# Optimization experiments

Measured on AMD Instinct MI355X. Metric: run time of the kernel, lower is better.

Reference implementation:

```python
import jax, jax.numpy as jnp
import numpy as np

T = 16384       # video length (frames)
C = 7           # out_features = d_model = num surgical phases
F_DIM = 2048    # mstcn_f_dim (spatial feature dim)
LEN_Q = 30      # sliding window length
N_HEADS = 4
D_K = 64        # attn_dim = min(64, mstcn_f_maps=64)
D_FF = 64       # d_ff = mstcn_f_maps


def setup_inputs() -> dict:
    key = jax.random.key(0)
    ks = jax.random.split(key, 10)
    w = lambda i, shape: jax.random.normal(ks[i], shape, jnp.float32) * 0.05
    return {
        "x": jax.random.normal(ks[0], (1, C, T), jnp.float32),
        "long_feature": jax.random.normal(ks[1], (1, T, F_DIM), jnp.float32),
        "W_fc": w(2, (C, F_DIM)),              # nn.Linear(mstcn_f_dim, out_features, bias=False)
        "W_q": w(3, (N_HEADS * D_K, C)),
        "W_k": w(4, (N_HEADS * D_K, C)),
        "W_v": w(5, (N_HEADS * D_K, C)),
        "W_o": w(6, (C, N_HEADS * D_K)),
        "ln1_g": jnp.ones((C,), jnp.float32),
        "ln1_b": jnp.zeros((C,), jnp.float32),
        "W_ff1": w(7, (D_FF, C)),
        "W_ff2": w(8, (C, D_FF)),
        "ln2_g": jnp.ones((C,), jnp.float32),
        "ln2_b": jnp.zeros((C,), jnp.float32),
    }


def layer_norm(x, g, b, eps=1e-5):
    mu = x.mean(-1, keepdims=True)
    var = ((x - mu) ** 2).mean(-1, keepdims=True)
    return (x - mu) * jax.lax.rsqrt(var + eps) * g + b


def reference(x, long_feature, W_fc, W_q, W_k, W_v, W_o, ln1_g, ln1_b, W_ff1, W_ff2, ln2_g, ln2_b):
    # --- vectorized sliding-window (replaces the Python loop of zeros/cat/stack) ---
    feats = x[0].T                                            # (T, C)
    padded = jnp.concatenate([jnp.zeros((LEN_Q - 1, C), feats.dtype), feats], axis=0)
    idx = jnp.arange(T)[:, None] + jnp.arange(LEN_Q)[None, :]  # window ends at frame i
    inputs = padded[idx]                                       # (T, LEN_Q, C)

    # --- spatial embedding: feas = tanh(fc(long_feature)).transpose(0,1) ---
    feas = jnp.tanh(long_feature[0] @ W_fc.T)[:, None, :]      # (T, 1, C)

    # --- decoder layer: cross MHA(query=feas, kv=inputs) + residual + LN ---
    q = (feas @ W_q.T).reshape(T, 1, N_HEADS, D_K).transpose(0, 2, 1, 3)       # (T,H,1,Dk)
    k = (inputs @ W_k.T).reshape(T, LEN_Q, N_HEADS, D_K).transpose(0, 2, 1, 3)  # (T,H,Lq,Dk)
    v = (inputs @ W_v.T).reshape(T, LEN_Q, N_HEADS, D_K).transpose(0, 2, 1, 3)  # (T,H,Lq,Dk)
    scores = jnp.einsum('thqd,thkd->thqk', q, k) / np.float32(np.sqrt(D_K))
    attn = jax.nn.softmax(scores, axis=-1)
    ctx = jnp.einsum('thqk,thkd->thqd', attn, v)
    ctx = ctx.transpose(0, 2, 1, 3).reshape(T, 1, N_HEADS * D_K)
    out = layer_norm(ctx @ W_o.T + feas, ln1_g, ln1_b)         # (T, 1, C)

    # --- position-wise FFN + residual + LN ---
    ff = jax.nn.relu(out @ W_ff1.T) @ W_ff2.T
    out = layer_norm(ff + out, ln2_g, ln2_b)
    return out[:, 0]                                           # (T, C) per-frame logits
```

## Files before the change

### kernel.cpp

```cpp
#include <hip/hip_runtime.h>
#include <math.h>

#define T_FRAMES 16384
#define FDIM 2048
#define LQ 30

__global__ __launch_bounds__(448) void setup_kernel(
    const float* __restrict__ Wq, const float* __restrict__ Wk,
    const float* __restrict__ Wv, const float* __restrict__ Wo,
    float* __restrict__ AM) {
  const int e = threadIdx.x;
  if (e >= 392) return;
  const int which = e / 196;
  const int r = e % 196;
  const int h = r / 49;
  const int rr = r % 49;
  const int c = rr / 7;
  const int c2 = rr % 7;
  float s = 0.0f;
  if (which == 0) {
    for (int d = 0; d < 64; ++d)
      s = fmaf(Wq[(h * 64 + d) * 7 + c], Wk[(h * 64 + d) * 7 + c2], s);
  } else {
    for (int d = 0; d < 64; ++d)
      s = fmaf(Wo[c * 256 + h * 64 + d], Wv[(h * 64 + d) * 7 + c2], s);
  }
  AM[e] = s;
}

#define FPB_A 8

__global__ __launch_bounds__(256) void feas_kernel(
    const float* __restrict__ lf,
    const float* __restrict__ Wfc,
    float* __restrict__ feas) {
  const int tid = threadIdx.x;
  const int lane = tid & 63;
  const int wave = tid >> 6;
  const int t0 = blockIdx.x * FPB_A + wave * 2;
  const float* lfp = lf + (size_t)t0 * FDIM + lane * 4;

  float4 a0[8], a1[8];
#pragma unroll
  for (int ch = 0; ch < 8; ++ch) a0[ch] = *(const float4*)(lfp + ch * 256);
#pragma unroll
  for (int ch = 0; ch < 8; ++ch) a1[ch] = *(const float4*)(lfp + FDIM + ch * 256);

  float acc0[7] = {0, 0, 0, 0, 0, 0, 0};
  float acc1[7] = {0, 0, 0, 0, 0, 0, 0};
#pragma unroll
  for (int ch = 0; ch < 8; ++ch) {
#pragma unroll
    for (int c = 0; c < 7; ++c) {
      const float4 w = *(const float4*)(Wfc + c * FDIM + ch * 256 + lane * 4);
      acc0[c] = fmaf(a0[ch].x, w.x, fmaf(a0[ch].y, w.y,
                fmaf(a0[ch].z, w.z, fmaf(a0[ch].w, w.w, acc0[c]))));
      acc1[c] = fmaf(a1[ch].x, w.x, fmaf(a1[ch].y, w.y,
                fmaf(a1[ch].z, w.z, fmaf(a1[ch].w, w.w, acc1[c]))));
    }
  }

#pragma unroll
  for (int c = 0; c < 7; ++c) {
    float v0 = acc0[c];
    float v1 = acc1[c];
#pragma unroll
    for (int off = 32; off > 0; off >>= 1) {
      v0 += __shfl_down(v0, off, 64);
      v1 += __shfl_down(v1, off, 64);
    }
    if (lane == 0) {
      feas[(size_t)t0 * 7 + c]       = tanhf(v0);
      feas[(size_t)(t0 + 1) * 7 + c] = tanhf(v1);
    }
  }
}

#define BF 64

__global__ __launch_bounds__(256) void attn_kernel(
    const float* __restrict__ x,
    const float* __restrict__ feas_g,
    const float* __restrict__ AM,
    const float* __restrict__ W1,
    const float* __restrict__ W2,
    const float* __restrict__ ln1g, const float* __restrict__ ln1b,
    const float* __restrict__ ln2g, const float* __restrict__ ln2b,
    float* __restrict__ out) {
  __shared__ float AM_s[392];
  __shared__ float ft[(BF + LQ - 1) * 7];
  __shared__ float feas_s[BF][7];
  __shared__ float hpart[BF][4][7];

  const int tid = threadIdx.x;
  const int t0 = blockIdx.x * BF;

  for (int i = tid; i < 392; i += 256) AM_s[i] = AM[i];
  for (int i = tid; i < (BF + LQ - 1) * 7; i += 256) {
    const int row = i / 7, c = i % 7;
    const int s = t0 - (LQ - 1) + row;
    ft[i] = (s >= 0) ? x[c * T_FRAMES + s] : 0.0f;
  }
  for (int i = tid; i < BF * 7; i += 256)
    feas_s[i / 7][i % 7] = feas_g[(size_t)t0 * 7 + i];
  __syncthreads();

  {
    const int f = tid >> 2;
    const int h = tid & 3;
    float fe[7];
#pragma unroll
    for (int c = 0; c < 7; ++c) fe[c] = feas_s[f][c];

    const float* Ah = AM_s + h * 49;
    const float* Mh = AM_s + 196 + h * 49;
    float qk[7];
#pragma unroll
    for (int c2 = 0; c2 < 7; ++c2) {
      float s = 0.0f;
#pragma unroll
      for (int c = 0; c < 7; ++c) s = fmaf(fe[c], Ah[c * 7 + c2], s);
      qk[c2] = s * 0.125f;
    }
    const float* frow = &ft[f * 7];
    float sc[LQ];
    float m = -1e30f;
#pragma unroll
    for (int j = 0; j < LQ; ++j) {
      const float* r = frow + j * 7;
      float s = 0.0f;
#pragma unroll
      for (int c2 = 0; c2 < 7; ++c2) s = fmaf(qk[c2], r[c2], s);
      sc[j] = s;
      m = fmaxf(m, s);
    }
    float sum = 0.0f;
    float wsum[7] = {0, 0, 0, 0, 0, 0, 0};
#pragma unroll
    for (int j = 0; j < LQ; ++j) {
      const float p = __expf(sc[j] - m);
      sum += p;
      const float* r = frow + j * 7;
#pragma unroll
      for (int c2 = 0; c2 < 7; ++c2) wsum[c2] = fmaf(p, r[c2], wsum[c2]);
    }
    const float inv = 1.0f / sum;
#pragma unroll
    for (int c = 0; c < 7; ++c) {
      float s = 0.0f;
#pragma unroll
      for (int c2 = 0; c2 < 7; ++c2) s = fmaf(Mh[c * 7 + c2], wsum[c2], s);
      hpart[f][h][c] = s * inv;
    }
  }
  __syncthreads();

  if (tid < BF) {
    const int f = tid;
    float v[7];
#pragma unroll
    for (int c = 0; c < 7; ++c)
      v[c] = feas_s[f][c] + hpart[f][0][c] + hpart[f][1][c] + hpart[f][2][c] + hpart[f][3][c];

    float mu = 0.0f;
#pragma unroll
    for (int c = 0; c < 7; ++c) mu += v[c];
    mu *= (1.0f / 7.0f);
    float var = 0.0f;
#pragma unroll
    for (int c = 0; c < 7; ++c) { const float d = v[c] - mu; var = fmaf(d, d, var); }
    var *= (1.0f / 7.0f);
    float rs = rsqrtf(var + 1e-5f);
    float o1[7];
#pragma unroll
    for (int c = 0; c < 7; ++c) o1[c] = (v[c] - mu) * rs * ln1g[c] + ln1b[c];

    float ff[7] = {0, 0, 0, 0, 0, 0, 0};
    for (int k = 0; k < 64; ++k) {
      float hk = 0.0f;
#pragma unroll
      for (int c = 0; c < 7; ++c) hk = fmaf(W1[k * 7 + c], o1[c], hk);
      hk = fmaxf(hk, 0.0f);
#pragma unroll
      for (int c = 0; c < 7; ++c) ff[c] = fmaf(W2[c * 64 + k], hk, ff[c]);
    }

#pragma unroll
    for (int c = 0; c < 7; ++c) v[c] = ff[c] + o1[c];
    mu = 0.0f;
#pragma unroll
    for (int c = 0; c < 7; ++c) mu += v[c];
    mu *= (1.0f / 7.0f);
    var = 0.0f;
#pragma unroll
    for (int c = 0; c < 7; ++c) { const float d = v[c] - mu; var = fmaf(d, d, var); }
    var *= (1.0f / 7.0f);
    rs = rsqrtf(var + 1e-5f);
    const int t = t0 + f;
#pragma unroll
    for (int c = 0; c < 7; ++c)
      out[(size_t)t * 7 + c] = (v[c] - mu) * rs * ln2g[c] + ln2b[c];
  }
}

extern "C" void kernel_launch(void* const* d_in, const int* in_sizes, int n_in,
                              void* d_out, int out_size, void* d_ws, size_t ws_size,
                              hipStream_t stream) {
  const float* x    = (const float*)d_in[0];
  const float* lf   = (const float*)d_in[1];
  const float* Wfc  = (const float*)d_in[2];
  const float* Wq   = (const float*)d_in[3];
  const float* Wk   = (const float*)d_in[4];
  const float* Wv   = (const float*)d_in[5];
  const float* Wo   = (const float*)d_in[6];
  const float* ln1g = (const float*)d_in[7];
  const float* ln1b = (const float*)d_in[8];
  const float* W1   = (const float*)d_in[9];
  const float* W2   = (const float*)d_in[10];
  const float* ln2g = (const float*)d_in[11];
  const float* ln2b = (const float*)d_in[12];
  float* out = (float*)d_out;

  float* AM = (float*)d_ws;

  setup_kernel<<<1, 448, 0, stream>>>(Wq, Wk, Wv, Wo, AM);
  feas_kernel<<<T_FRAMES / FPB_A, 256, 0, stream>>>(lf, Wfc, out);
  attn_kernel<<<T_FRAMES / BF, 256, 0, stream>>>(
      x, out, AM, W1, W2, ln1g, ln1b, ln2g, ln2b, out);
}
```

Measured before the change: 277.3 us.

## Fuse feature projection into attention kernel with Wfc staged in LDS

Merges the long-feature projection kernel into the attention/FFN kernel. Each block of 32 frames now computes its own tanh(fc) features into shared memory, which removes the global round-trip of feas and one kernel launch. The 57KB Wfc matrix is copied into LDS per block instead of being read from global/L2 by every wave. The trade-off is that the large LDS allocation limits occupancy, and each of the 512 blocks reloads Wfc, on a kernel that is bound by HBM streaming of long_feature.

```diff
diff --git a/kernel.cpp b/kernel.cpp
--- a/kernel.cpp
+++ b/kernel.cpp
@@ -4,6 +4,8 @@
 #define T_FRAMES 16384
 #define FDIM 2048
 #define LQ 30
+#define BF 32
+#define ITERS 4
 
 __global__ __launch_bounds__(448) void setup_kernel(
     const float* __restrict__ Wq, const float* __restrict__ Wk,
@@ -28,84 +30,82 @@
   AM[e] = s;
 }
 
-#define FPB_A 8
-
-__global__ __launch_bounds__(256) void feas_kernel(
+__global__ __launch_bounds__(256) void fused_kernel(
     const float* __restrict__ lf,
     const float* __restrict__ Wfc,
-    float* __restrict__ feas) {
-  const int tid = threadIdx.x;
-  const int lane = tid & 63;
-  const int wave = tid >> 6;
-  const int t0 = blockIdx.x * FPB_A + wave * 2;
-  const float* lfp = lf + (size_t)t0 * FDIM + lane * 4;
-
-  float4 a0[8], a1[8];
-#pragma unroll
-  for (int ch = 0; ch < 8; ++ch) a0[ch] = *(const float4*)(lfp + ch * 256);
-#pragma unroll
-  for (int ch = 0; ch < 8; ++ch) a1[ch] = *(const float4*)(lfp + FDIM + ch * 256);
-
-  float acc0[7] = {0, 0, 0, 0, 0, 0, 0};
-  float acc1[7] = {0, 0, 0, 0, 0, 0, 0};
-#pragma unroll
-  for (int ch = 0; ch < 8; ++ch) {
-#pragma unroll
-    for (int c = 0; c < 7; ++c) {
-      const float4 w = *(const float4*)(Wfc + c * FDIM + ch * 256 + lane * 4);
-      acc0[c] = fmaf(a0[ch].x, w.x, fmaf(a0[ch].y, w.y,
-                fmaf(a0[ch].z, w.z, fmaf(a0[ch].w, w.w, acc0[c]))));
-      acc1[c] = fmaf(a1[ch].x, w.x, fmaf(a1[ch].y, w.y,
-                fmaf(a1[ch].z, w.z, fmaf(a1[ch].w, w.w, acc1[c]))));
-    }
-  }
-
-#pragma unroll
-  for (int c = 0; c < 7; ++c) {
-    float v0 = acc0[c];
-    float v1 = acc1[c];
-#pragma unroll
-    for (int off = 32; off > 0; off >>= 1) {
-      v0 += __shfl_down(v0, off, 64);
-      v1 += __shfl_down(v1, off, 64);
-    }
-    if (lane == 0) {
-      feas[(size_t)t0 * 7 + c]       = tanhf(v0);
-      feas[(size_t)(t0 + 1) * 7 + c] = tanhf(v1);
-    }
-  }
-}
-
-#define BF 64
-
-__global__ __launch_bounds__(256) void attn_kernel(
     const float* __restrict__ x,
-    const float* __restrict__ feas_g,
     const float* __restrict__ AM,
     const float* __restrict__ W1,
     const float* __restrict__ W2,
     const float* __restrict__ ln1g, const float* __restrict__ ln1b,
     const float* __restrict__ ln2g, const float* __restrict__ ln2b,
     float* __restrict__ out) {
+  __shared__ float wfc_s[7 * FDIM];
   __shared__ float AM_s[392];
   __shared__ float ft[(BF + LQ - 1) * 7];
   __shared__ float feas_s[BF][7];
   __shared__ float hpart[BF][4][7];
 
   const int tid = threadIdx.x;
+  const int lane = tid & 63;
+  const int wave = tid >> 6;
   const int t0 = blockIdx.x * BF;
 
+  {
+    const float4* src = (const float4*)Wfc;
+    float4* dst = (float4*)wfc_s;
+    for (int i = tid; i < (7 * FDIM) / 4; i += 256) dst[i] = src[i];
+  }
   for (int i = tid; i < 392; i += 256) AM_s[i] = AM[i];
   for (int i = tid; i < (BF + LQ - 1) * 7; i += 256) {
     const int row = i / 7, c = i % 7;
     const int s = t0 - (LQ - 1) + row;
     ft[i] = (s >= 0) ? x[c * T_FRAMES + s] : 0.0f;
   }
-  for (int i = tid; i < BF * 7; i += 256)
-    feas_s[i / 7][i % 7] = feas_g[(size_t)t0 * 7 + i];
   __syncthreads();
 
-  {
+  for (int it = 0; it < ITERS; ++it) {
+    const int fl = it * 8 + wave * 2;
+    const float* lfp = lf + (size_t)(t0 + fl) * FDIM + lane * 4;
+
+    float4 a0[8], a1[8];
+#pragma unroll
+    for (int ch = 0; ch < 8; ++ch) a0[ch] = *(const float4*)(lfp + ch * 256);
+#pragma unroll
+    for (int ch = 0; ch < 8; ++ch) a1[ch] = *(const float4*)(lfp + FDIM + ch * 256);
+
+    float acc0[7] = {0, 0, 0, 0, 0, 0, 0};
+    float acc1[7] = {0, 0, 0, 0, 0, 0, 0};
+#pragma unroll
+    for (int ch = 0; ch < 8; ++ch) {
+#pragma unroll
+      for (int c = 0; c < 7; ++c) {
+        const float4 w = *(const float4*)(&wfc_s[c * FDIM + ch * 256 + lane * 4]);
+        acc0[c] = fmaf(a0[ch].x, w.x, fmaf(a0[ch].y, w.y,
+                  fmaf(a0[ch].z, w.z, fmaf(a0[ch].w, w.w, acc0[c]))));
+        acc1[c] = fmaf(a1[ch].x, w.x, fmaf(a1[ch].y, w.y,
+                  fmaf(a1[ch].z, w.z, fmaf(a1[ch].w, w.w, acc1[c]))));
+      }
+    }
+
+#pragma unroll
+    for (int c = 0; c < 7; ++c) {
+      float v0 = acc0[c];
+      float v1 = acc1[c];
+#pragma unroll
+      for (int off = 32; off > 0; off >>= 1) {
+        v0 += __shfl_down(v0, off, 64);
+        v1 += __shfl_down(v1, off, 64);
+      }
+      if (lane == 0) {
+        feas_s[fl][c]     = tanhf(v0);
+        feas_s[fl + 1][c] = tanhf(v1);
+      }
+    }
+  }
+  __syncthreads();
+
+  if (tid < BF * 4) {
     const int f = tid >> 2;
     const int h = tid & 3;
     float fe[7];
@@ -224,7 +224,6 @@
   float* AM = (float*)d_ws;
 
   setup_kernel<<<1, 448, 0, stream>>>(Wq, Wk, Wv, Wo, AM);
-  feas_kernel<<<T_FRAMES / FPB_A, 256, 0, stream>>>(lf, Wfc, out);
-  attn_kernel<<<T_FRAMES / BF, 256, 0, stream>>>(
-      x, out, AM, W1, W2, ln1g, ln1b, ln2g, ln2b, out);
+  fused_kernel<<<T_FRAMES / BF, 256, 0, stream>>>(
+      lf, Wfc, x, AM, W1, W2, ln1g, ln1b, ln2g, ln2b, out);
 }
```

New measurement: 268.7 us. 1.03x faster.

## Tile feas GEMV through double-buffered swizzled LDS with register prefetch

Applied to the files above, without the earlier changes.

Rewrites the spatial-feature projection so each block handles 64 frames, staging 128-column chunks of long_feature into double-buffered, XOR-swizzled shared memory while the next chunk is prefetched into registers. Each thread owns one frame and a quarter of each chunk and reads Wfc with wave-uniform addresses, then partial sums are reduced through shared memory instead of wave shuffles. The aim is better overlap of the 128MB streaming read with compute and fewer W loads per frame. In exchange it uses many more registers, large LDS and two barriers per chunk pair, and launches only 256 blocks, which may limit occupancy and bandwidth.

```diff
diff --git a/kernel.cpp b/kernel.cpp
--- a/kernel.cpp
+++ b/kernel.cpp
@@ -4,6 +4,10 @@
 #define T_FRAMES 16384
 #define FDIM 2048
 #define LQ 30
+#define CHK 128
+#define NCHK (FDIM / CHK)
+#define FT 64
+#define BF 64
 
 __global__ __launch_bounds__(448) void setup_kernel(
     const float* __restrict__ Wq, const float* __restrict__ Wk,
@@ -28,55 +32,97 @@
   AM[e] = s;
 }
 
-#define FPB_A 8
-
 __global__ __launch_bounds__(256) void feas_kernel(
     const float* __restrict__ lf,
     const float* __restrict__ Wfc,
     float* __restrict__ feas) {
+  __shared__ float lfs[2][FT * CHK];
+  __shared__ float red[4][FT * 7];
+
   const int tid = threadIdx.x;
-  const int lane = tid & 63;
-  const int wave = tid >> 6;
-  const int t0 = blockIdx.x * FPB_A + wave * 2;
-  const float* lfp = lf + (size_t)t0 * FDIM + lane * 4;
-
-  float4 a0[8], a1[8];
-#pragma unroll
-  for (int ch = 0; ch < 8; ++ch) a0[ch] = *(const float4*)(lfp + ch * 256);
-#pragma unroll
-  for (int ch = 0; ch < 8; ++ch) a1[ch] = *(const float4*)(lfp + FDIM + ch * 256);
-
-  float acc0[7] = {0, 0, 0, 0, 0, 0, 0};
-  float acc1[7] = {0, 0, 0, 0, 0, 0, 0};
-#pragma unroll
-  for (int ch = 0; ch < 8; ++ch) {
-#pragma unroll
-    for (int c = 0; c < 7; ++c) {
-      const float4 w = *(const float4*)(Wfc + c * FDIM + ch * 256 + lane * 4);
-      acc0[c] = fmaf(a0[ch].x, w.x, fmaf(a0[ch].y, w.y,
-                fmaf(a0[ch].z, w.z, fmaf(a0[ch].w, w.w, acc0[c]))));
-      acc1[c] = fmaf(a1[ch].x, w.x, fmaf(a1[ch].y, w.y,
-                fmaf(a1[ch].z, w.z, fmaf(a1[ch].w, w.w, acc1[c]))));
-    }
-  }
-
-#pragma unroll
-  for (int c = 0; c < 7; ++c) {
-    float v0 = acc0[c];
-    float v1 = acc1[c];
-#pragma unroll
-    for (int off = 32; off > 0; off >>= 1) {
-      v0 += __shfl_down(v0, off, 64);
-      v1 += __shfl_down(v1, off, 64);
-    }
-    if (lane == 0) {
-      feas[(size_t)t0 * 7 + c]       = tanhf(v0);
-      feas[(size_t)(t0 + 1) * 7 + c] = tanhf(v1);
-    }
-  }
-}
-
-#define BF 64
+  const int f   = tid & 63;
+  const int q   = tid >> 6;
+  const int t0  = blockIdx.x * FT;
+  const float* lfbase = lf + (size_t)t0 * FDIM;
+
+  int gofs[8];
+  int lofs[8];
+#pragma unroll
+  for (int p = 0; p < 8; ++p) {
+    const int i = p * 256 + tid, r = i >> 5, g = i & 31;
+    gofs[p] = r * FDIM + g * 4;
+    lofs[p] = r * CHK + (((g * 16) ^ ((r & 31) << 4)) >> 2);
+  }
+  int rofs[8];
+#pragma unroll
+  for (int j = 0; j < 8; ++j) {
+    const int x = q * 8 + j;
+    rofs[j] = f * CHK + ((((x * 16)) ^ ((f & 31) << 4)) >> 2);
+  }
+
+  const int qk = __builtin_amdgcn_readfirstlane(q) * 32;
+
+  float4 bankA[8], bankB[8];
+
+#pragma unroll
+  for (int p = 0; p < 8; ++p) bankA[p] = *(const float4*)(lfbase + gofs[p]);
+#pragma unroll
+  for (int p = 0; p < 8; ++p) *(float4*)(&lfs[0][lofs[p]]) = bankA[p];
+#pragma unroll
+  for (int p = 0; p < 8; ++p) bankB[p] = *(const float4*)(lfbase + gofs[p] + CHK);
+  __syncthreads();
+
+  float acc[7] = {0, 0, 0, 0, 0, 0, 0};
+
+#define COMPUTE_CHUNK(PB, CH)                                                  \
+  {                                                                            \
+    float4 a[8];                                                               \
+    _Pragma("unroll") for (int j = 0; j < 8; ++j)                              \
+        a[j] = *(const float4*)(&lfs[PB][rofs[j]]);                            \
+    const float* wrow = Wfc + (CH) * CHK + qk;                                 \
+    _Pragma("unroll") for (int c = 0; c < 7; ++c) {                            \
+      const float4* wp = (const float4*)(wrow + c * FDIM);                     \
+      _Pragma("unroll") for (int j = 0; j < 8; ++j) {                          \
+        const float4 w = wp[j];                                                \
+        acc[c] = fmaf(a[j].x, w.x, fmaf(a[j].y, w.y,                           \
+                 fmaf(a[j].z, w.z, fmaf(a[j].w, w.w, acc[c]))));               \
+      }                                                                        \
+    }                                                                          \
+  }
+
+  for (int ch2 = 0; ch2 < NCHK / 2; ++ch2) {
+    const int ch = ch2 * 2;
+    const bool more = (ch2 < NCHK / 2 - 1);
+    if (more) {
+#pragma unroll
+      for (int p = 0; p < 8; ++p)
+        bankA[p] = *(const float4*)(lfbase + gofs[p] + (ch + 2) * CHK);
+    }
+    COMPUTE_CHUNK(0, ch)
+#pragma unroll
+    for (int p = 0; p < 8; ++p) *(float4*)(&lfs[1][lofs[p]]) = bankB[p];
+    __syncthreads();
+    if (more) {
+#pragma unroll
+      for (int p = 0; p < 8; ++p)
+        bankB[p] = *(const float4*)(lfbase + gofs[p] + (ch + 3) * CHK);
+    }
+    COMPUTE_CHUNK(1, ch + 1)
+    if (more) {
+#pragma unroll
+      for (int p = 0; p < 8; ++p) *(float4*)(&lfs[0][lofs[p]]) = bankA[p];
+    }
+    __syncthreads();
+  }
+
+#pragma unroll
+  for (int c = 0; c < 7; ++c) red[q][f * 7 + c] = acc[c];
+  __syncthreads();
+  for (int j = tid; j < FT * 7; j += 256) {
+    const float s = red[0][j] + red[1][j] + red[2][j] + red[3][j];
+    feas[(size_t)t0 * 7 + j] = tanhf(s);
+  }
+}
 
 __global__ __launch_bounds__(256) void attn_kernel(
     const float* __restrict__ x,
@@ -224,7 +270,7 @@
   float* AM = (float*)d_ws;
 
   setup_kernel<<<1, 448, 0, stream>>>(Wq, Wk, Wv, Wo, AM);
-  feas_kernel<<<T_FRAMES / FPB_A, 256, 0, stream>>>(lf, Wfc, out);
+  feas_kernel<<<T_FRAMES / FT, 256, 0, stream>>>(lf, Wfc, out);
   attn_kernel<<<T_FRAMES / BF, 256, 0, stream>>>(
       x, out, AM, W1, W2, ln1g, ln1b, ln2g, ln2b, out);
 }
```

Result: slower. 321.3 us (+15.9%).

## Stage W_fc in LDS and split the feature reduction across waves per frame

Applied to the files above, without the earlier changes.

The feature-projection kernel now copies the whole 7x2048 W_fc into shared memory once per block of 32 frames. Each lane owns one frame and one quarter-half slice of the 2048-wide dot product. Partial sums are combined with a cross-half shuffle and a shared-memory reduction across waves before tanh. This removes the repeated global/L1 reads of W_fc for every pair of frames. In exchange, the 56KB of LDS per block limits occupancy, and each lane reads a different row, so global loads are less coalesced.

```diff
diff --git a/kernel.cpp b/kernel.cpp
--- a/kernel.cpp
+++ b/kernel.cpp
@@ -4,6 +4,8 @@
 #define T_FRAMES 16384
 #define FDIM 2048
 #define LQ 30
+#define FB 32
+#define BF 64
 
 __global__ __launch_bounds__(448) void setup_kernel(
     const float* __restrict__ Wq, const float* __restrict__ Wk,
@@ -28,55 +30,71 @@
   AM[e] = s;
 }
 
-#define FPB_A 8
-
 __global__ __launch_bounds__(256) void feas_kernel(
     const float* __restrict__ lf,
     const float* __restrict__ Wfc,
     float* __restrict__ feas) {
-  const int tid = threadIdx.x;
+  __shared__ float wfc_s[7 * FDIM];
+  __shared__ float red[4][FB * 7];
+
+  const int tid  = threadIdx.x;
   const int lane = tid & 63;
   const int wave = tid >> 6;
-  const int t0 = blockIdx.x * FPB_A + wave * 2;
-  const float* lfp = lf + (size_t)t0 * FDIM + lane * 4;
-
-  float4 a0[8], a1[8];
-#pragma unroll
-  for (int ch = 0; ch < 8; ++ch) a0[ch] = *(const float4*)(lfp + ch * 256);
-#pragma unroll
-  for (int ch = 0; ch < 8; ++ch) a1[ch] = *(const float4*)(lfp + FDIM + ch * 256);
-
-  float acc0[7] = {0, 0, 0, 0, 0, 0, 0};
-  float acc1[7] = {0, 0, 0, 0, 0, 0, 0};
-#pragma unroll
-  for (int ch = 0; ch < 8; ++ch) {
+  const int half = lane >> 5;
+  const int f    = lane & 31;
+  const int t0   = blockIdx.x * FB;
+
+  {
+    const float4* src = (const float4*)Wfc;
+    float4* dst = (float4*)wfc_s;
+#pragma unroll
+    for (int i = 0; i < 14; ++i) dst[tid + i * 256] = src[tid + i * 256];
+  }
+  __syncthreads();
+
+  const int kb = wave * 512 + half * 256;
+  const float* rowp  = lf + (size_t)(t0 + f) * FDIM + kb;
+  const float* wbase = wfc_s + kb;
+
+  float acc[7] = {0, 0, 0, 0, 0, 0, 0};
+
+  for (int j = 0; j < 64; j += 4) {
+    const float4 a0 = *(const float4*)(rowp + j * 4);
+    const float4 a1 = *(const float4*)(rowp + j * 4 + 4);
+    const float4 a2 = *(const float4*)(rowp + j * 4 + 8);
+    const float4 a3 = *(const float4*)(rowp + j * 4 + 12);
 #pragma unroll
     for (int c = 0; c < 7; ++c) {
-      const float4 w = *(const float4*)(Wfc + c * FDIM + ch * 256 + lane * 4);
-      acc0[c] = fmaf(a0[ch].x, w.x, fmaf(a0[ch].y, w.y,
-                fmaf(a0[ch].z, w.z, fmaf(a0[ch].w, w.w, acc0[c]))));
-      acc1[c] = fmaf(a1[ch].x, w.x, fmaf(a1[ch].y, w.y,
-                fmaf(a1[ch].z, w.z, fmaf(a1[ch].w, w.w, acc1[c]))));
-    }
-  }
-
-#pragma unroll
-  for (int c = 0; c < 7; ++c) {
-    float v0 = acc0[c];
-    float v1 = acc1[c];
-#pragma unroll
-    for (int off = 32; off > 0; off >>= 1) {
-      v0 += __shfl_down(v0, off, 64);
-      v1 += __shfl_down(v1, off, 64);
-    }
-    if (lane == 0) {
-      feas[(size_t)t0 * 7 + c]       = tanhf(v0);
-      feas[(size_t)(t0 + 1) * 7 + c] = tanhf(v1);
-    }
-  }
-}
-
-#define BF 64
+      const float* wc = wbase + c * FDIM + j * 4;
+      const float4 w0 = *(const float4*)(wc);
+      const float4 w1 = *(const float4*)(wc + 4);
+      const float4 w2 = *(const float4*)(wc + 8);
+      const float4 w3 = *(const float4*)(wc + 12);
+      acc[c] = fmaf(a0.x, w0.x, fmaf(a0.y, w0.y,
+               fmaf(a0.z, w0.z, fmaf(a0.w, w0.w, acc[c]))));
+      acc[c] = fmaf(a1.x, w1.x, fmaf(a1.y, w1.y,
+               fmaf(a1.z, w1.z, fmaf(a1.w, w1.w, acc[c]))));
+      acc[c] = fmaf(a2.x, w2.x, fmaf(a2.y, w2.y,
+               fmaf(a2.z, w2.z, fmaf(a2.w, w2.w, acc[c]))));
+      acc[c] = fmaf(a3.x, w3.x, fmaf(a3.y, w3.y,
+               fmaf(a3.z, w3.z, fmaf(a3.w, w3.w, acc[c]))));
+    }
+  }
+
+#pragma unroll
+  for (int c = 0; c < 7; ++c) acc[c] += __shfl_xor(acc[c], 32, 64);
+
+  if (lane < 32) {
+#pragma unroll
+    for (int c = 0; c < 7; ++c) red[wave][f * 7 + c] = acc[c];
+  }
+  __syncthreads();
+
+  for (int j = tid; j < FB * 7; j += 256) {
+    const float s = red[0][j] + red[1][j] + red[2][j] + red[3][j];
+    feas[(size_t)t0 * 7 + j] = tanhf(s);
+  }
+}
 
 __global__ __launch_bounds__(256) void attn_kernel(
     const float* __restrict__ x,
@@ -224,7 +242,7 @@
   float* AM = (float*)d_ws;
 
   setup_kernel<<<1, 448, 0, stream>>>(Wq, Wk, Wv, Wo, AM);
-  feas_kernel<<<T_FRAMES / FPB_A, 256, 0, stream>>>(lf, Wfc, out);
+  feas_kernel<<<T_FRAMES / FB, 256, 0, stream>>>(lf, Wfc, out);
   attn_kernel<<<T_FRAMES / BF, 256, 0, stream>>>(
       x, out, AM, W1, W2, ln1g, ln1b, ln2g, ln2b, out);
 }
```

New measurement: 250.2 us. 1.11x faster.
